# Kernel optimization log

Hardware: AMD Instinct MI355X
Metric: run time of the kernel (lower is better)

Reference implementation:

```python
import jax, jax.numpy as jnp
import numpy as np
import math

B, L, H, NH = 8, 512, 512, 8
DH = H // NH


def setup_inputs() -> dict:
    key = jax.random.key(0)
    ks = jax.random.split(key, 12)
    src = jax.random.normal(ks[0], (B, L, H), dtype=jnp.float32)
    seq_len = jax.random.randint(ks[1], (B,), L // 2, L + 1).astype(jnp.int32)
    seq_len = seq_len.at[0].set(L)  # guarantee max(seq_len) == L
    pe = jax.random.normal(ks[2], (2 * L, H), dtype=jnp.float32) * 0.02
    s = 1.0 / math.sqrt(H)
    Wq = jax.random.normal(ks[3], (H, H), dtype=jnp.float32) * s
    bq = jnp.zeros((H,), jnp.float32)
    Wk = jax.random.normal(ks[4], (H, H), dtype=jnp.float32) * s
    bk = jnp.zeros((H,), jnp.float32)
    Wv = jax.random.normal(ks[5], (H, H), dtype=jnp.float32) * s
    bv = jnp.zeros((H,), jnp.float32)
    Wr = jax.random.normal(ks[6], (H, H), dtype=jnp.float32) * s
    br = jnp.zeros((H,), jnp.float32)
    u = jax.random.normal(ks[7], (NH, DH), dtype=jnp.float32) * 0.02
    v = jax.random.normal(ks[8], (NH, DH), dtype=jnp.float32) * 0.02
    gamma = jnp.ones((H,), jnp.float32)
    beta = jnp.zeros((H,), jnp.float32)
    return dict(src=src, seq_len=seq_len, pe=pe, Wq=Wq, bq=bq, Wk=Wk, bk=bk,
                Wv=Wv, bv=bv, Wr=Wr, br=br, u=u, v=v, gamma=gamma, beta=beta)


def reference(src, seq_len, pe, Wq, bq, Wk, bk, Wv, bv, Wr, br, u, v, gamma, beta):
    b, l, h = src.shape
    dh = h // NH
    # relative distance rel[i,j] = j - i, lookup pe[rel + L]  -> [L, L, H]
    rel = jnp.arange(l)[None, :] - jnp.arange(l)[:, None]
    R = pe[rel + l]
    # projections (torch Linear: y = x W^T + b)
    q = src @ Wq.T + bq
    k = src @ Wk.T + bk
    val = src @ Wv.T + bv
    R = R @ Wr.T + br
    # split heads
    q = q.reshape(b, l, NH, dh)
    k = k.reshape(b, l, NH, dh)
    val = val.reshape(b, l, NH, dh)
    R = R.reshape(l, l, NH, dh)
    # Transformer-XL score terms
    A = jnp.einsum('bihd,bjhd->bhij', q, k)
    Bt = jnp.einsum('bihd,ijhd->bhij', q, R)
    C = jnp.einsum('hd,bjhd->bhj', u, k)[:, :, None, :]
    D = jnp.einsum('ijhd,hd->hij', R, v)[None]
    scores = (A + Bt + C + D) / math.sqrt(dh)
    # key-side padding mask
    mask = jnp.arange(l)[None, :] < seq_len[:, None]  # [B, L]
    scores = jnp.where(mask[:, None, None, :], scores, jnp.float32(-1e15))
    attn = jax.nn.softmax(scores, axis=-1)
    out = jnp.einsum('bhij,bjhd->bihd', attn, val).reshape(b, l, h)
    res = src + out
    # LayerNorm (eps=1e-5) then exact GELU
    mu = jnp.mean(res, axis=-1, keepdims=True)
    var = jnp.mean((res - mu) ** 2, axis=-1, keepdims=True)
    ln = (res - mu) * jax.lax.rsqrt(var + 1e-5) * gamma + beta
    return jax.nn.gelu(ln, approximate=False)
```

## Files before the change

kernel.cpp:

```cpp
#include <hip/hip_runtime.h>
#include <math.h>

#define Bn 8
#define Ln 512
#define Hn 512
#define NHn 8
#define DHn 64

typedef __attribute__((ext_vector_type(8))) short short8;
typedef __attribute__((ext_vector_type(4))) float f32x4;

__device__ __forceinline__ unsigned short f2bf(float f) {
    unsigned int u = __float_as_uint(f);
    unsigned int r = (u + 0x7FFFu + ((u >> 16) & 1u)) >> 16;
    return (unsigned short)r;
}
__device__ __forceinline__ float bf2f(unsigned short s) {
    return __uint_as_float(((unsigned int)s) << 16);
}

__device__ __forceinline__ void gload_lds16(const void* g, void* l) {
    __builtin_amdgcn_global_load_lds(
        (const __attribute__((address_space(1))) unsigned int*)g,
        (__attribute__((address_space(3))) unsigned int*)l,
        16, 0, 0);
}

__global__ __launch_bounds__(256) void convert_kernel(
    const float* __restrict__ src, const float* __restrict__ pe,
    const float* __restrict__ Wq, const float* __restrict__ Wk,
    const float* __restrict__ Wv, const float* __restrict__ Wr,
    const float* __restrict__ bq, const float* __restrict__ bk,
    const float* __restrict__ bv,
    unsigned short* __restrict__ src_bf, unsigned short* __restrict__ pe_bf,
    unsigned short* __restrict__ Wcat_bf, unsigned short* __restrict__ Wr_bf,
    float* __restrict__ bcat)
{
    const int bid = blockIdx.x;
    const int tid = threadIdx.x;
    const float* in; unsigned short* outp; int base4;
    if (bid < 2048)      { in = src; outp = src_bf;           base4 = bid; }
    else if (bid < 2560) { in = pe;  outp = pe_bf;            base4 = bid - 2048; }
    else if (bid < 2816) { in = Wq;  outp = Wcat_bf;          base4 = bid - 2560; }
    else if (bid < 3072) { in = Wk;  outp = Wcat_bf + 262144; base4 = bid - 2816; }
    else if (bid < 3328) { in = Wv;  outp = Wcat_bf + 524288; base4 = bid - 3072; }
    else if (bid < 3584) { in = Wr;  outp = Wr_bf;            base4 = bid - 3328; }
    else {
        const int idx = (bid - 3584) * 256 + tid;
        if (idx < 512)            bcat[idx] = bq[idx];
        else if (idx < 1024)      bcat[idx] = bk[idx - 512];
        else if (idx < 1536)      bcat[idx] = bv[idx - 1024];
        return;
    }
    const int i4 = (base4 * 256 + tid) * 4;
    float4 x = *(const float4*)&in[i4];
    ushort4 o;
    o.x = f2bf(x.x); o.y = f2bf(x.y); o.z = f2bf(x.z); o.w = f2bf(x.w);
    *(ushort4*)&outp[i4] = o;
}

__global__ __launch_bounds__(256) void gemm_kernel(
    const unsigned short* __restrict__ src_bf,
    const unsigned short* __restrict__ Wcat_bf,
    const unsigned short* __restrict__ pe_bf,
    const unsigned short* __restrict__ Wr_bf,
    const float* __restrict__ bcat, const float* __restrict__ br,
    unsigned short* __restrict__ QKb,
    unsigned short* __restrict__ VTg,
    unsigned short* __restrict__ Rpb)
{
    const int bid = blockIdx.x;
    int mode, m0, n0;
    const unsigned short *A, *B;
    if (bid < 256) {
        mode = 0; n0 = (bid & 7) * 128; m0 = (bid >> 3) * 128;
        A = src_bf + (size_t)m0 * 512;
        B = Wcat_bf + (size_t)n0 * 512;
    } else if (bid < 384) {
        mode = 1; m0 = ((bid - 256) & 3) * 128; n0 = ((bid - 256) >> 2) * 128;
        A = Wcat_bf + (size_t)(1024 + m0) * 512;
        B = src_bf + (size_t)n0 * 512;
    } else {
        mode = 2; n0 = ((bid - 384) & 3) * 128; m0 = ((bid - 384) >> 2) * 128;
        A = pe_bf + (size_t)m0 * 512;
        B = Wr_bf + (size_t)n0 * 512;
    }

    __shared__ unsigned short As[128 * 32];
    __shared__ unsigned short Bs[128 * 32];

    const int t = threadIdx.x;
    const int wave = t >> 6, lane = t & 63;
    const int wm = (wave >> 1) * 64;
    const int wn = (wave & 1) * 64;

    f32x4 acc[4][4] = {};

    const int srow = wave * 32 + (lane >> 2);
    const int scol = (lane & 3) * 8;
    const unsigned short* Ag = A + (size_t)srow * 512 + scol;
    const unsigned short* Bg = B + (size_t)srow * 512 + scol;
    unsigned short* AsW = &As[srow * 32 + scol];
    unsigned short* BsW = &Bs[srow * 32 + scol];

    for (int k0 = 0; k0 < 512; k0 += 32) {
        __syncthreads();
        gload_lds16(Ag + k0,            AsW);
        gload_lds16(Ag + k0 + 16 * 512, AsW + 16 * 32);
        gload_lds16(Bg + k0,            BsW);
        gload_lds16(Bg + k0 + 16 * 512, BsW + 16 * 32);
        __syncthreads();

        short8 af[4], bf[4];
        #pragma unroll
        for (int mt = 0; mt < 4; ++mt)
            af[mt] = *(const short8*)&As[(wm + mt * 16 + (lane & 15)) * 32 + (lane >> 4) * 8];
        #pragma unroll
        for (int nt = 0; nt < 4; ++nt)
            bf[nt] = *(const short8*)&Bs[(wn + nt * 16 + (lane & 15)) * 32 + (lane >> 4) * 8];
        #pragma unroll
        for (int mt = 0; mt < 4; ++mt)
            #pragma unroll
            for (int nt = 0; nt < 4; ++nt)
                acc[mt][nt] = __builtin_amdgcn_mfma_f32_16x16x32_bf16(
                    af[mt], bf[nt], acc[mt][nt], 0, 0, 0);
    }

    const int crow = (lane >> 4) * 4;
    const int ccol = lane & 15;
    if (mode == 0) {
        #pragma unroll
        for (int mt = 0; mt < 4; ++mt)
            #pragma unroll
            for (int nt = 0; nt < 4; ++nt) {
                const int n = n0 + wn + nt * 16 + ccol;
                const float bn = bcat[n];
                #pragma unroll
                for (int r = 0; r < 4; ++r) {
                    const int m = m0 + wm + mt * 16 + crow + r;
                    QKb[(size_t)m * 1024 + n] = f2bf(acc[mt][nt][r] + bn);
                }
            }
    } else if (mode == 1) {
        #pragma unroll
        for (int mt = 0; mt < 4; ++mt)
            #pragma unroll
            for (int nt = 0; nt < 4; ++nt) {
                const int n = n0 + wn + nt * 16 + ccol;
                #pragma unroll
                for (int r = 0; r < 4; ++r) {
                    const int dv = m0 + wm + mt * 16 + crow + r;
                    VTg[(size_t)dv * 4096 + n] = f2bf(acc[mt][nt][r] + bcat[1024 + dv]);
                }
            }
    } else {
        #pragma unroll
        for (int mt = 0; mt < 4; ++mt)
            #pragma unroll
            for (int nt = 0; nt < 4; ++nt) {
                const int n = n0 + wn + nt * 16 + ccol;
                const float bn = br[n];
                #pragma unroll
                for (int r = 0; r < 4; ++r) {
                    const int m = m0 + wm + mt * 16 + crow + r;
                    Rpb[(size_t)m * 512 + n] = f2bf(acc[mt][nt][r] + bn);
                }
            }
    }
}

#define PADK 72
#define QRS 133
__global__ __launch_bounds__(256) void attn_kernel(
    const unsigned short* __restrict__ QKb,
    const unsigned short* __restrict__ VTg,
    const unsigned short* __restrict__ Rpb,
    const float* __restrict__ u, const float* __restrict__ v,
    const int* __restrict__ seq_len, unsigned short* __restrict__ Ob)
{
    const int i0 = blockIdx.x * 64;
    const int h  = blockIdx.y;
    const int b  = blockIdx.z;
    const int slen = seq_len[b];

    __shared__ unsigned short k_s [64 * PADK];
    __shared__ unsigned short vT_s[64 * PADK];
    __shared__ unsigned short rs_s[64 * PADK];
    __shared__ unsigned short p_s [64 * PADK];
    __shared__ unsigned short qrT [64 * QRS];

    const int t = threadIdx.x;
    const int wave = t >> 6, lane = t & 63;
    const int l = lane & 15, g = lane >> 4;

    short8 af_qu[2], af_qv[2];
    {
        const unsigned short* qrow =
            QKb + (size_t)(b * 512 + i0 + wave * 16 + l) * 1024 + h * 64;
        #pragma unroll
        for (int kk = 0; kk < 2; ++kk) {
            const int c = kk * 32 + g * 8;
            unsigned short q8[8];
            *(uint4*)q8 = *(const uint4*)(qrow + c);
            float4 u0 = *(const float4*)(u + h * 64 + c);
            float4 u1 = *(const float4*)(u + h * 64 + c + 4);
            float4 v0 = *(const float4*)(v + h * 64 + c);
            float4 v1 = *(const float4*)(v + h * 64 + c + 4);
            float uf[8] = {u0.x,u0.y,u0.z,u0.w,u1.x,u1.y,u1.z,u1.w};
            float vf[8] = {v0.x,v0.y,v0.z,v0.w,v1.x,v1.y,v1.z,v1.w};
            short8 qu, qv;
            #pragma unroll
            for (int e = 0; e < 8; ++e) {
                float qf = bf2f(q8[e]);
                qu[e] = (short)f2bf(qf + uf[e]);
                qv[e] = (short)f2bf(qf + vf[e]);
            }
            af_qu[kk] = qu; af_qv[kk] = qv;
        }
    }

    float m_run[4], l_run[4];
    f32x4 accO[4] = {};
    #pragma unroll
    for (int r = 0; r < 4; ++r) { m_run[r] = -3.0e38f; l_run[r] = 0.f; }

    const int jr = t >> 2, c0 = (t & 3) * 16;

    auto btChunk = [&](int slot0) {
        #pragma unroll
        for (int nt8 = 0; nt8 < 4; ++nt8) {
            f32x4 a = {};
            #pragma unroll
            for (int kk = 0; kk < 2; ++kk) {
                short8 br8 = *(const short8*)&rs_s[(nt8 * 16 + l) * PADK + kk * 32 + g * 8];
                a = __builtin_amdgcn_mfma_f32_16x16x32_bf16(af_qv[kk], br8, a, 0, 0, 0);
            }
            const int sl = slot0 + nt8 * 16 + l;
            #pragma unroll
            for (int r = 0; r < 4; ++r)
                qrT[(wave * 16 + g * 4 + r) * QRS + sl] = f2bf(a[r]);
        }
    };

    const unsigned short* rpA = Rpb + (size_t)(448 - i0 + jr) * 512 + h * 64 + c0;
    uint4 rA0 = *(const uint4*)(rpA);
    uint4 rA1 = *(const uint4*)(rpA + 8);
    const unsigned short* kp0 = QKb + (size_t)(b * 512 + jr) * 1024 + 512 + h * 64 + c0;
    uint4 kc0 = *(const uint4*)(kp0), kc1 = *(const uint4*)(kp0 + 8);
    const unsigned short* vp0 = VTg + (size_t)(h * 64 + jr) * 4096 + b * 512 + c0;
    uint4 vc0 = *(const uint4*)(vp0), vc1 = *(const uint4*)(vp0 + 8);
    const unsigned short* rp0 = Rpb + (size_t)(512 - i0 + jr) * 512 + h * 64 + c0;
    uint4 rc0 = *(const uint4*)(rp0), rc1 = *(const uint4*)(rp0 + 8);

    *(uint4*)(rs_s + jr * PADK + c0)     = rA0;
    *(uint4*)(rs_s + jr * PADK + c0 + 8) = rA1;
    __syncthreads();
    btChunk((448 - i0) & 127);

    for (int jt = 0; jt < 8; ++jt) {
        const int j0 = jt * 64;
        __syncthreads();

        *(uint4*)(k_s  + jr * PADK + c0)     = kc0;
        *(uint4*)(k_s  + jr * PADK + c0 + 8) = kc1;
        *(uint4*)(vT_s + jr * PADK + c0)     = vc0;
        *(uint4*)(vT_s + jr * PADK + c0 + 8) = vc1;
        *(uint4*)(rs_s + jr * PADK + c0)     = rc0;
        *(uint4*)(rs_s + jr * PADK + c0 + 8) = rc1;
        __syncthreads();

        if (jt < 7) {
            const unsigned short* kp =
                QKb + (size_t)(b * 512 + j0 + 64 + jr) * 1024 + 512 + h * 64 + c0;
            kc0 = *(const uint4*)(kp); kc1 = *(const uint4*)(kp + 8);
            const unsigned short* vp =
                VTg + (size_t)(h * 64 + jr) * 4096 + b * 512 + j0 + 64 + c0;
            vc0 = *(const uint4*)(vp); vc1 = *(const uint4*)(vp + 8);
            const unsigned short* rp =
                Rpb + (size_t)(j0 + 64 - i0 + 512 + jr) * 512 + h * 64 + c0;
            rc0 = *(const uint4*)(rp); rc1 = *(const uint4*)(rp + 8);
        }

        btChunk((j0 - i0 + 512) & 127);

        f32x4 accA[4];
        #pragma unroll
        for (int nt = 0; nt < 4; ++nt) {
            f32x4 a = {};
            #pragma unroll
            for (int kk = 0; kk < 2; ++kk) {
                short8 bk8 = *(const short8*)&k_s[(nt * 16 + l) * PADK + kk * 32 + g * 8];
                a = __builtin_amdgcn_mfma_f32_16x16x32_bf16(af_qu[kk], bk8, a, 0, 0, 0);
            }
            accA[nt] = a;
        }

        float sv[4][4];
        #pragma unroll
        for (int nt = 0; nt < 4; ++nt)
            #pragma unroll
            for (int r = 0; r < 4; ++r) {
                const int il = wave * 16 + g * 4 + r;
                const int slot = (j0 + nt * 16 + l - i0 - il + 512) & 127;
                const float qr = bf2f(qrT[il * QRS + slot]);
                float s = (accA[nt][r] + qr) * 0.125f;
                if (j0 + nt * 16 + l >= slen) s = -1e15f;
                sv[nt][r] = s;
            }

        float alpha_r[4];
        #pragma unroll
        for (int r = 0; r < 4; ++r) {
            float tm = fmaxf(fmaxf(sv[0][r], sv[1][r]), fmaxf(sv[2][r], sv[3][r]));
            tm = fmaxf(tm, __shfl_xor(tm, 1, 64));
            tm = fmaxf(tm, __shfl_xor(tm, 2, 64));
            tm = fmaxf(tm, __shfl_xor(tm, 4, 64));
            tm = fmaxf(tm, __shfl_xor(tm, 8, 64));
            const float mn = fmaxf(m_run[r], tm);
            alpha_r[r] = __expf(m_run[r] - mn);
            m_run[r] = mn;
            float ss = 0.f;
            #pragma unroll
            for (int nt = 0; nt < 4; ++nt) {
                const float pe_ = __expf(sv[nt][r] - mn);
                sv[nt][r] = pe_; ss += pe_;
            }
            ss += __shfl_xor(ss, 1, 64);
            ss += __shfl_xor(ss, 2, 64);
            ss += __shfl_xor(ss, 4, 64);
            ss += __shfl_xor(ss, 8, 64);
            l_run[r] = l_run[r] * alpha_r[r] + ss;
        }

        #pragma unroll
        for (int nt = 0; nt < 4; ++nt)
            #pragma unroll
            for (int r = 0; r < 4; ++r)
                p_s[(wave * 16 + g * 4 + r) * PADK + nt * 16 + l] = f2bf(sv[nt][r]);

        #pragma unroll
        for (int nt = 0; nt < 4; ++nt)
            #pragma unroll
            for (int r = 0; r < 4; ++r)
                accO[nt][r] *= alpha_r[r];

        short8 pa[2];
        #pragma unroll
        for (int kk = 0; kk < 2; ++kk)
            pa[kk] = *(const short8*)&p_s[(wave * 16 + l) * PADK + kk * 32 + g * 8];
        #pragma unroll
        for (int nt = 0; nt < 4; ++nt) {
            #pragma unroll
            for (int kk = 0; kk < 2; ++kk) {
                short8 bv8 = *(const short8*)&vT_s[(nt * 16 + l) * PADK + kk * 32 + g * 8];
                accO[nt] = __builtin_amdgcn_mfma_f32_16x16x32_bf16(pa[kk], bv8, accO[nt], 0, 0, 0);
            }
        }
    }

    float inv[4];
    #pragma unroll
    for (int r = 0; r < 4; ++r) inv[r] = 1.0f / l_run[r];
    #pragma unroll
    for (int nt = 0; nt < 4; ++nt)
        #pragma unroll
        for (int r = 0; r < 4; ++r)
            Ob[(size_t)(b * 512 + i0 + wave * 16 + g * 4 + r) * 512 + h * 64 + nt * 16 + l]
                = f2bf(accO[nt][r] * inv[r]);
}

__global__ __launch_bounds__(256) void ln_gelu_kernel(
    const float* __restrict__ src, const unsigned short* __restrict__ Ob,
    const float* __restrict__ gamma, const float* __restrict__ beta,
    float* __restrict__ out)
{
    const int row  = blockIdx.x * 4 + (threadIdx.x >> 6);
    const int lane = threadIdx.x & 63;
    const int c0   = lane * 8;
    const float* s = &src[(size_t)row * 512 + c0];
    float4 s0 = *(const float4*)(s);
    float4 s1 = *(const float4*)(s + 4);
    unsigned short o8[8];
    *(uint4*)o8 = *(const uint4*)(Ob + (size_t)row * 512 + c0);
    float x[8];
    x[0] = s0.x + bf2f(o8[0]); x[1] = s0.y + bf2f(o8[1]);
    x[2] = s0.z + bf2f(o8[2]); x[3] = s0.w + bf2f(o8[3]);
    x[4] = s1.x + bf2f(o8[4]); x[5] = s1.y + bf2f(o8[5]);
    x[6] = s1.z + bf2f(o8[6]); x[7] = s1.w + bf2f(o8[7]);
    float sum = 0.f;
    #pragma unroll
    for (int e = 0; e < 8; ++e) sum += x[e];
    #pragma unroll
    for (int off = 32; off >= 1; off >>= 1) sum += __shfl_xor(sum, off, 64);
    const float mean = sum * (1.0f / 512.0f);
    float var = 0.f;
    #pragma unroll
    for (int e = 0; e < 8; ++e) { float d = x[e] - mean; var += d * d; }
    #pragma unroll
    for (int off = 32; off >= 1; off >>= 1) var += __shfl_xor(var, off, 64);
    var *= (1.0f / 512.0f);
    const float inv = rsqrtf(var + 1e-5f);
    float4 g0 = *(const float4*)(gamma + c0);
    float4 g1 = *(const float4*)(gamma + c0 + 4);
    float4 b0 = *(const float4*)(beta + c0);
    float4 b1 = *(const float4*)(beta + c0 + 4);
    float gm[8] = {g0.x,g0.y,g0.z,g0.w,g1.x,g1.y,g1.z,g1.w};
    float bt[8] = {b0.x,b0.y,b0.z,b0.w,b1.x,b1.y,b1.z,b1.w};
    float r8[8];
    #pragma unroll
    for (int e = 0; e < 8; ++e) {
        float ln = (x[e] - mean) * inv * gm[e] + bt[e];
        r8[e] = 0.5f * ln * (1.0f + erff(ln * 0.70710678118654752f));
    }
    float* op = &out[(size_t)row * 512 + c0];
    *(float4*)(op)     = make_float4(r8[0], r8[1], r8[2], r8[3]);
    *(float4*)(op + 4) = make_float4(r8[4], r8[5], r8[6], r8[7]);
}

extern "C" void kernel_launch(void* const* d_in, const int* in_sizes, int n_in,
                              void* d_out, int out_size, void* d_ws, size_t ws_size,
                              hipStream_t stream)
{
    const float* src     = (const float*)d_in[0];
    const int*   seq_len = (const int*)  d_in[1];
    const float* pe      = (const float*)d_in[2];
    const float* Wq      = (const float*)d_in[3];
    const float* bq      = (const float*)d_in[4];
    const float* Wk      = (const float*)d_in[5];
    const float* bk      = (const float*)d_in[6];
    const float* Wv      = (const float*)d_in[7];
    const float* bv      = (const float*)d_in[8];
    const float* Wr      = (const float*)d_in[9];
    const float* br      = (const float*)d_in[10];
    const float* u       = (const float*)d_in[11];
    const float* v       = (const float*)d_in[12];
    const float* gamma   = (const float*)d_in[13];
    const float* beta    = (const float*)d_in[14];
    float* out = (float*)d_out;

    char* w = (char*)d_ws;
    unsigned short* QKb     = (unsigned short*)(w);
    unsigned short* VTg     = (unsigned short*)(w + 8388608);
    unsigned short* Rpb     = (unsigned short*)(w + 12582912);
    unsigned short* Ob      = (unsigned short*)(w + 13631488);
    unsigned short* src_bf  = (unsigned short*)(w + 17825792);
    unsigned short* pe_bf   = (unsigned short*)(w + 22020096);
    unsigned short* Wcat_bf = (unsigned short*)(w + 23068672);
    unsigned short* Wr_bf   = (unsigned short*)(w + 24641536);
    float*          bcat    = (float*)         (w + 25165824);

    convert_kernel<<<dim3(3590), 256, 0, stream>>>(
        src, pe, Wq, Wk, Wv, Wr, bq, bk, bv,
        src_bf, pe_bf, Wcat_bf, Wr_bf, bcat);

    gemm_kernel<<<dim3(416), 256, 0, stream>>>(
        src_bf, Wcat_bf, pe_bf, Wr_bf, bcat, br, QKb, VTg, Rpb);

    attn_kernel<<<dim3(8, NHn, Bn), 256, 0, stream>>>(QKb, VTg, Rpb, u, v, seq_len, Ob);

    ln_gelu_kernel<<<dim3(Bn * Ln / 4), 256, 0, stream>>>(src, Ob, gamma, beta, out);
}
```

Before: 137.6 us.

## Skip masked key tiles, transpose qr buffer, register-staged GEMM loads

The attention loop now runs only over key tiles up to the batch's sequence length instead of all eight. Fully masked tiles contribute exp(-1e15 - m) = 0, so skipping them leaves the result unchanged and removes their MFMA, softmax and load work. The relative-position score buffer is transposed so each lane writes four values with one vector store instead of four scalar stores. The projection GEMM replaces direct global-to-LDS loads with register-staged prefetch of the next k-slice, which overlaps global latency with compute but raises register pressure.

```diff
diff --git a/kernel.cpp b/kernel.cpp
--- a/kernel.cpp
+++ b/kernel.cpp
@@ -17,13 +17,6 @@
 }
 __device__ __forceinline__ float bf2f(unsigned short s) {
     return __uint_as_float(((unsigned int)s) << 16);
-}
-
-__device__ __forceinline__ void gload_lds16(const void* g, void* l) {
-    __builtin_amdgcn_global_load_lds(
-        (const __attribute__((address_space(1))) unsigned int*)g,
-        (__attribute__((address_space(3))) unsigned int*)l,
-        16, 0, 0);
 }
 
 __global__ __launch_bounds__(256) void convert_kernel(
@@ -103,13 +96,25 @@
     unsigned short* AsW = &As[srow * 32 + scol];
     unsigned short* BsW = &Bs[srow * 32 + scol];
 
+    uint4 a0 = *(const uint4*)(Ag);
+    uint4 a1 = *(const uint4*)(Ag + 16 * 512);
+    uint4 b0 = *(const uint4*)(Bg);
+    uint4 b1 = *(const uint4*)(Bg + 16 * 512);
+
     for (int k0 = 0; k0 < 512; k0 += 32) {
         __syncthreads();
-        gload_lds16(Ag + k0,            AsW);
-        gload_lds16(Ag + k0 + 16 * 512, AsW + 16 * 32);
-        gload_lds16(Bg + k0,            BsW);
-        gload_lds16(Bg + k0 + 16 * 512, BsW + 16 * 32);
+        *(uint4*)(AsW)           = a0;
+        *(uint4*)(AsW + 16 * 32) = a1;
+        *(uint4*)(BsW)           = b0;
+        *(uint4*)(BsW + 16 * 32) = b1;
         __syncthreads();
+
+        if (k0 + 32 < 512) {
+            a0 = *(const uint4*)(Ag + k0 + 32);
+            a1 = *(const uint4*)(Ag + k0 + 32 + 16 * 512);
+            b0 = *(const uint4*)(Bg + k0 + 32);
+            b1 = *(const uint4*)(Bg + k0 + 32 + 16 * 512);
+        }
 
         short8 af[4], bf[4];
         #pragma unroll
@@ -170,7 +175,6 @@
 }
 
 #define PADK 72
-#define QRS 133
 __global__ __launch_bounds__(256) void attn_kernel(
     const unsigned short* __restrict__ QKb,
     const unsigned short* __restrict__ VTg,
@@ -182,12 +186,13 @@
     const int h  = blockIdx.y;
     const int b  = blockIdx.z;
     const int slen = seq_len[b];
+    const int njt = (slen + 63) >> 6;
 
     __shared__ unsigned short k_s [64 * PADK];
     __shared__ unsigned short vT_s[64 * PADK];
     __shared__ unsigned short rs_s[64 * PADK];
     __shared__ unsigned short p_s [64 * PADK];
-    __shared__ unsigned short qrT [64 * QRS];
+    __shared__ unsigned short qrTT[128 * 72];
 
     const int t = threadIdx.x;
     const int wave = t >> 6, lane = t & 63;
@@ -236,9 +241,9 @@
                 a = __builtin_amdgcn_mfma_f32_16x16x32_bf16(af_qv[kk], br8, a, 0, 0, 0);
             }
             const int sl = slot0 + nt8 * 16 + l;
-            #pragma unroll
-            for (int r = 0; r < 4; ++r)
-                qrT[(wave * 16 + g * 4 + r) * QRS + sl] = f2bf(a[r]);
+            ushort4 w4;
+            w4.x = f2bf(a[0]); w4.y = f2bf(a[1]); w4.z = f2bf(a[2]); w4.w = f2bf(a[3]);
+            *(ushort4*)(qrTT + sl * 72 + wave * 16 + g * 4) = w4;
         }
     };
 
@@ -257,7 +262,7 @@
     __syncthreads();
     btChunk((448 - i0) & 127);
 
-    for (int jt = 0; jt < 8; ++jt) {
+    for (int jt = 0; jt < njt; ++jt) {
         const int j0 = jt * 64;
         __syncthreads();
 
@@ -269,7 +274,7 @@
         *(uint4*)(rs_s + jr * PADK + c0 + 8) = rc1;
         __syncthreads();
 
-        if (jt < 7) {
+        if (jt + 1 < njt) {
             const unsigned short* kp =
                 QKb + (size_t)(b * 512 + j0 + 64 + jr) * 1024 + 512 + h * 64 + c0;
             kc0 = *(const uint4*)(kp); kc1 = *(const uint4*)(kp + 8);
@@ -302,7 +307,7 @@
             for (int r = 0; r < 4; ++r) {
                 const int il = wave * 16 + g * 4 + r;
                 const int slot = (j0 + nt * 16 + l - i0 - il + 512) & 127;
-                const float qr = bf2f(qrT[il * QRS + slot]);
+                const float qr = bf2f(qrTT[slot * 72 + il]);
                 float s = (accA[nt][r] + qr) * 0.125f;
                 if (j0 + nt * 16 + l >= slen) s = -1e15f;
                 sv[nt][r] = s;
```

Result: faster. 133.6 us (-2.9%).
